# Kernel optimization log

Hardware: AMD Instinct MI355X
Metric: run time of the kernel (lower is better)

Reference implementation:

```python
import jax, jax.numpy as jnp
import numpy as np
import math

H = 1024
N_HEADS = 16
B, S = 2, 2048

def setup_inputs() -> dict:
    key = jax.random.key(0)
    ks = jax.random.split(key, 10)
    s = 0.02
    inp = {
        "x": jax.random.normal(ks[0], (B, S, H), dtype=jnp.float32),
        "attention_mask": jnp.zeros((B, 1, 1, S), dtype=jnp.float32),
        "Wq": jax.random.normal(ks[1], (H, H), dtype=jnp.float32) * s,
        "bq": jnp.zeros((H,), dtype=jnp.float32),
        "Wk": jax.random.normal(ks[2], (H, H), dtype=jnp.float32) * s,
        "bk": jnp.zeros((H,), dtype=jnp.float32),
        "Wv": jax.random.normal(ks[3], (H, H), dtype=jnp.float32) * s,
        "bv": jnp.zeros((H,), dtype=jnp.float32),
        "Wo": jax.random.normal(ks[4], (H, H), dtype=jnp.float32) * s,
        "bo": jnp.zeros((H,), dtype=jnp.float32),
    }
    return inp

def reference(x, attention_mask, Wq, bq, Wk, bk, Wv, bv, Wo, bo):
    b, s, h = x.shape
    n = N_HEADS
    d = h // n
    scale = 1.0 / math.sqrt(h / n)
    # Linear projections (torch Linear: x @ W.T + b)
    q = (x @ Wq.T + bq).reshape(b, s, n, d).transpose(0, 2, 1, 3)  # [b,n,s,d]
    k = (x @ Wk.T + bk).reshape(b, s, n, d).transpose(0, 2, 1, 3)
    v = (x @ Wv.T + bv).reshape(b, s, n, d).transpose(0, 2, 1, 3)
    scores = jnp.einsum("bnqd,bnkd->bnqk", q, k) * scale + attention_mask
    probs = jax.nn.softmax(scores, axis=-1)
    attn = jnp.einsum("bnqk,bnkd->bnqd", probs, v)
    attn = attn.transpose(0, 2, 1, 3).reshape(b, s, h)
    return attn @ Wo.T + bo
```

## Files before the change

kernel.cpp:

```cpp
#include <hip/hip_runtime.h>

typedef __bf16 bf16;
typedef __bf16 bf16x8 __attribute__((ext_vector_type(8)));
typedef __bf16 bf16x4 __attribute__((ext_vector_type(4)));
typedef float f32x4 __attribute__((ext_vector_type(4)));
typedef float f32x16 __attribute__((ext_vector_type(16)));
typedef unsigned int u32;
typedef u32 u32x4 __attribute__((ext_vector_type(4)));
typedef const u32 __attribute__((address_space(1)))* gp1_t;
typedef u32 __attribute__((address_space(3)))* lp3_t;

constexpr int Hdim = 1024;
constexpr int SEQ  = 2048;
constexpr int NB   = 2;
constexpr int NHEAD = 16;
constexpr int DHEAD = 64;
constexpr int MR = NB * SEQ;
constexpr float LOG2E = 1.4426950408889634f;
constexpr float QSCALE = 0.125f * LOG2E;

__device__ __forceinline__ float fexp2(float x) { return __builtin_amdgcn_exp2f(x); }

__device__ __forceinline__ void gld16(const void* g, void* l) {
  __builtin_amdgcn_global_load_lds((gp1_t)g, (lp3_t)l, 16, 0, 0);
}

__device__ __forceinline__ u32 cvtpk_bf16(float lo, float hi) {
  u32 r;
  asm("v_cvt_pk_bf16_f32 %0, %1, %2" : "=v"(r) : "v"(lo), "v"(hi));
  return r;
}

__global__ __launch_bounds__(256) void cvt_all_k(
    const float* __restrict__ x, const float* __restrict__ Wq, const float* __restrict__ Wk,
    const float* __restrict__ Wv, const float* __restrict__ Wo, const float* __restrict__ mask,
    bf16* __restrict__ xb, bf16* __restrict__ wqkv, bf16* __restrict__ wob,
    float* __restrict__ maskS) {
  const int n8x = MR * Hdim / 8;
  const int n8w = Hdim * Hdim / 8;
  int i = blockIdx.x * 256 + threadIdx.x;
  if (i >= n8x + 4 * n8w) {
    int o = i - (n8x + 4 * n8w);
    const float4* p = reinterpret_cast<const float4*>(mask) + (size_t)o * 2;
    float4 a = p[0], b = p[1];
    a.x *= LOG2E; a.y *= LOG2E; a.z *= LOG2E; a.w *= LOG2E;
    b.x *= LOG2E; b.y *= LOG2E; b.z *= LOG2E; b.w *= LOG2E;
    float4* q = reinterpret_cast<float4*>(maskS) + (size_t)o * 2;
    q[0] = a; q[1] = b;
    return;
  }
  const float* src;
  bf16* dst;
  int slot;
  if (i < n8x) {
    src = x; dst = xb; slot = i;
  } else {
    int j = i - n8x;
    int w = j >> 17;
    int o = j & (n8w - 1);
    if (w == 0)      { src = Wq; dst = wqkv;            }
    else if (w == 1) { src = Wk; dst = wqkv + (size_t)Hdim * Hdim;     }
    else if (w == 2) { src = Wv; dst = wqkv + (size_t)2 * Hdim * Hdim; }
    else             { src = Wo; dst = wob;             }
    slot = o;
  }
  const float4* p = reinterpret_cast<const float4*>(src) + (size_t)slot * 2;
  float4 a = p[0], b = p[1];
  bf16x8 o8;
  o8[0] = (bf16)a.x; o8[1] = (bf16)a.y; o8[2] = (bf16)a.z; o8[3] = (bf16)a.w;
  o8[4] = (bf16)b.x; o8[5] = (bf16)b.y; o8[6] = (bf16)b.z; o8[7] = (bf16)b.w;
  reinterpret_cast<bf16x8*>(dst)[slot] = o8;
}

__global__ __launch_bounds__(256) void qkv_gemm_k(
    const bf16* __restrict__ A, const bf16* __restrict__ Bw,
    const float* __restrict__ bq, const float* __restrict__ bk, const float* __restrict__ bv,
    bf16* __restrict__ Qw, bf16* __restrict__ Kw, bf16* __restrict__ VTw)
{
  __shared__ __align__(16) bf16 As[3][128][32];
  __shared__ __align__(16) bf16 Bs[3][128][32];

  const int t = threadIdx.x;
  const int lane = t & 63, wave = t >> 6;
  const int ql = lane & 15, g = lane >> 4;
  const int wr = wave >> 1, wc = wave & 1;
  const int row0 = blockIdx.x * 128;
  const int col0 = blockIdx.y * 128;
  const int z = blockIdx.y >> 3;
  const float* bias = (z == 0) ? bq : (z == 1) ? bk : bv;
  const int rsl = (g ^ ((ql >> 1) & 3)) * 8;

  f32x4 acc[4][4] = {};

#define STAGE_QKV(buf, kt)                                                        \
  {                                                                               \
    _Pragma("unroll")                                                             \
    for (int i = 0; i < 2; ++i) {                                                 \
      int c = i * 256 + t;                                                        \
      int r = c >> 2, sp = c & 3;                                                 \
      int sl = (sp ^ ((r >> 1) & 3)) << 3;                                        \
      gld16(&A[(size_t)(row0 + r) * Hdim + (kt) + sl], (char*)&As[buf][0][0] + c * 16); \
      gld16(&Bw[(size_t)(col0 + r) * Hdim + (kt) + sl], (char*)&Bs[buf][0][0] + c * 16); \
    }                                                                             \
  }

  constexpr int NT = Hdim / 32;
  STAGE_QKV(0, 0);
  STAGE_QKV(1, 32);

  int cur = 0;
  for (int it = 0; it < NT; ++it) {
    if (it + 2 < NT) {
      int stg = cur + 2; if (stg >= 3) stg -= 3;
      STAGE_QKV(stg, (it + 2) * 32);
      asm volatile("s_waitcnt vmcnt(8)" ::: "memory");
    } else if (it + 1 < NT) {
      asm volatile("s_waitcnt vmcnt(4)" ::: "memory");
    } else {
      asm volatile("s_waitcnt vmcnt(0)" ::: "memory");
    }
    __builtin_amdgcn_s_barrier();

    bf16x8 af[4], bfr[4];
#pragma unroll
    for (int m = 0; m < 4; ++m)
      af[m] = *reinterpret_cast<const bf16x8*>(&As[cur][wr * 64 + m * 16 + ql][rsl]);
#pragma unroll
    for (int n = 0; n < 4; ++n)
      bfr[n] = *reinterpret_cast<const bf16x8*>(&Bs[cur][wc * 64 + n * 16 + ql][rsl]);
#pragma unroll
    for (int m = 0; m < 4; ++m)
#pragma unroll
      for (int n = 0; n < 4; ++n)
        acc[m][n] = __builtin_amdgcn_mfma_f32_16x16x32_bf16(af[m], bfr[n], acc[m][n], 0, 0, 0);

    __builtin_amdgcn_s_barrier();
    cur = (cur + 1 == 3) ? 0 : cur + 1;
  }
#undef STAGE_QKV

  const float oscale = (z == 0) ? QSCALE : 1.0f;
#pragma unroll
  for (int m = 0; m < 4; ++m) {
#pragma unroll
    for (int n = 0; n < 4; ++n) {
#pragma unroll
      for (int r = 0; r < 4; ++r) {
        int gi = row0 + wr * 64 + m * 16 + g * 4 + r;
        int gj = col0 + wc * 64 + n * 16 + ql;
        int j1 = gj & (Hdim - 1);
        float v = (acc[m][n][r] + bias[j1]) * oscale;
        int b = gi >> 11, s = gi & (SEQ - 1);
        int hh = j1 >> 6, dd = j1 & 63;
        if (z == 0)
          Qw[((size_t)(b * NHEAD + hh) * SEQ + s) * DHEAD + dd] = (bf16)v;
        else if (z == 1)
          Kw[((size_t)(b * NHEAD + hh) * SEQ + s) * DHEAD + dd] = (bf16)v;
        else
          VTw[((size_t)(b * NHEAD + hh) * DHEAD + dd) * SEQ + s] = (bf16)v;
      }
    }
  }
}

__global__ __launch_bounds__(256, 2) void attn_fwd_k(
    const bf16* __restrict__ Q, const bf16* __restrict__ K,
    const bf16* __restrict__ VT, const float* __restrict__ maskS,
    bf16* __restrict__ Out)
{
  const int head = blockIdx.x;
  const int qt = blockIdx.y;
  const int b = head >> 4;
  const int hh = head & 15;
  const int t = threadIdx.x, lane = t & 63, wave = t >> 6;
  const int q = lane & 31, h = lane >> 5;

  __shared__ __align__(16) bf16 Ks[3][64][64];
  __shared__ __align__(16) bf16 VTs[3][64][64];
  __shared__ __align__(16) float Ms[SEQ];

  const bf16* Qh  = Q  + (size_t)head * SEQ * DHEAD;
  const bf16* Kh  = K  + (size_t)head * SEQ * DHEAD;
  const bf16* VTh = VT + (size_t)head * DHEAD * SEQ;
  const float* mrow = maskS + (size_t)b * SEQ;

  const int q0w = qt * 128 + wave * 32;

  bf16x8 qf[4];
#pragma unroll
  for (int s = 0; s < 4; ++s)
    qf[s] = *reinterpret_cast<const bf16x8*>(&Qh[(size_t)(q0w + q) * DHEAD + s * 16 + 8 * h]);

  f32x16 accT[2] = {};
  f32x4 psum4 = {0.f, 0.f, 0.f, 0.f};

#define STAGE_KV(buf, tile)                                                       \
  {                                                                               \
    const int nb0 = (tile) * 64;                                                  \
    _Pragma("unroll")                                                             \
    for (int i = 0; i < 2; ++i) {                                                 \
      int c = i * 256 + t, r = c >> 3, sp = c & 7, sl = sp ^ (r & 7);             \
      gld16(&Kh[(size_t)(nb0 + r) * DHEAD + sl * 8], (char*)&Ks[buf][0][0] + c * 16); \
      gld16(&VTh[(size_t)r * SEQ + nb0 + sl * 8], (char*)&VTs[buf][0][0] + c * 16);   \
    }                                                                             \
  }

  constexpr int NT = SEQ / 64;
#pragma unroll
  for (int i = 0; i < 2; ++i) {
    int c = i * 256 + t;
    gld16(&mrow[c * 4], (char*)&Ms[0] + c * 16);
  }
  STAGE_KV(0, 0);
  STAGE_KV(1, 1);
  asm volatile("s_waitcnt vmcnt(4)" ::: "memory");
  __builtin_amdgcn_s_barrier();

  int cur = 0;
  for (int it = 0; it < NT; ++it) {
    if (it + 2 < NT) {
      int stg = cur + 2; if (stg >= 3) stg -= 3;
      STAGE_KV(stg, it + 2);
    }

    const char* ksb = (const char*)&Ks[cur][0][0];
    const char* vsb = (const char*)&VTs[cur][0][0];
    const int kb0 = it * 64;

    f32x16 sacc[2];
#pragma unroll
    for (int tt = 0; tt < 2; ++tt) {
#pragma unroll
      for (int s = 0; s < 4; ++s) {
        f32x4 m4 = *reinterpret_cast<const f32x4*>(&Ms[kb0 + 32 * tt + 8 * s + 4 * h]);
#pragma unroll
        for (int r = 0; r < 4; ++r) sacc[tt][s * 4 + r] = m4[r];
      }
    }

    __builtin_amdgcn_s_setprio(1);
#pragma unroll
    for (int tt = 0; tt < 2; ++tt) {
      const int row = 32 * tt + q;
      const int rsw = (row & 7) << 4;
#pragma unroll
      for (int s = 0; s < 4; ++s) {
        bf16x8 kf = *reinterpret_cast<const bf16x8*>(ksb + row * 128 + ((32 * s + 16 * h) ^ rsw));
        sacc[tt] = __builtin_amdgcn_mfma_f32_32x32x16_bf16(kf, qf[s], sacc[tt], 0, 0, 0);
      }
    }
    __builtin_amdgcn_s_setprio(0);

    float pe[2][16];
#pragma unroll
    for (int tt = 0; tt < 2; ++tt)
#pragma unroll
      for (int i = 0; i < 16; ++i) {
        pe[tt][i] = fexp2(sacc[tt][i]);
        psum4[i & 3] += pe[tt][i];
      }

    u32x4 pw[4];
#pragma unroll
    for (int m = 0; m < 4; ++m) {
      const int tt = m >> 1, mi = (m & 1) * 8;
      u32 w0a = cvtpk_bf16(pe[tt][mi + 0], pe[tt][mi + 1]);
      u32 w0b = cvtpk_bf16(pe[tt][mi + 2], pe[tt][mi + 3]);
      u32 w1a = cvtpk_bf16(pe[tt][mi + 4], pe[tt][mi + 5]);
      u32 w1b = cvtpk_bf16(pe[tt][mi + 6], pe[tt][mi + 7]);
      asm("v_permlane32_swap_b32 %0, %1" : "+v"(w0a), "+v"(w1a));
      asm("v_permlane32_swap_b32 %0, %1" : "+v"(w0b), "+v"(w1b));
      pw[m][0] = w0a; pw[m][1] = w0b; pw[m][2] = w1a; pw[m][3] = w1b;
    }

    __builtin_amdgcn_s_setprio(1);
#pragma unroll
    for (int td = 0; td < 2; ++td) {
      const int row = 32 * td + q;
      const int rsw = (row & 7) << 4;
#pragma unroll
      for (int m = 0; m < 4; ++m) {
        bf16x8 vf = *reinterpret_cast<const bf16x8*>(vsb + row * 128 + ((32 * m + 16 * h) ^ rsw));
        bf16x8 pf = __builtin_bit_cast(bf16x8, pw[m]);
        accT[td] = __builtin_amdgcn_mfma_f32_32x32x16_bf16(vf, pf, accT[td], 0, 0, 0);
      }
    }
    __builtin_amdgcn_s_setprio(0);

    if (it + 2 < NT)      asm volatile("s_waitcnt vmcnt(4)" ::: "memory");
    else if (it + 1 < NT) asm volatile("s_waitcnt vmcnt(0)" ::: "memory");
    __builtin_amdgcn_s_barrier();
    cur = (cur + 1 == 3) ? 0 : cur + 1;
  }
#undef STAGE_KV

  float l = (psum4[0] + psum4[1]) + (psum4[2] + psum4[3]);
  l += __shfl_xor(l, 32);
  const float inv = 1.0f / l;

  char* slab = (char*)&Ks[0][0][0] + wave * 4096;
  const int qsw = (q & 7) << 4;
#pragma unroll
  for (int td = 0; td < 2; ++td)
#pragma unroll
    for (int s = 0; s < 4; ++s) {
      bf16x4 o4;
#pragma unroll
      for (int r = 0; r < 4; ++r) o4[r] = (bf16)(accT[td][s * 4 + r] * inv);
      *reinterpret_cast<bf16x4*>(slab + q * 128 + (((32 * td + 8 * s + 4 * h) * 2) ^ qsw)) = o4;
    }
  asm volatile("s_waitcnt lgkmcnt(0)" ::: "memory");
#pragma unroll
  for (int i = 0; i < 4; ++i) {
    const int row = i * 8 + (lane >> 3);
    bf16x8 v = *reinterpret_cast<const bf16x8*>(slab + row * 128 + (((lane & 7) << 4) ^ ((row & 7) << 4)));
    *reinterpret_cast<bf16x8*>(&Out[((size_t)(b * SEQ) + q0w + row) * Hdim + hh * 64 + (lane & 7) * 8]) = v;
  }
}

__global__ __launch_bounds__(256) void out_gemm_k(
    const bf16* __restrict__ A, const bf16* __restrict__ Bm,
    const float* __restrict__ bias, float* __restrict__ C)
{
  __shared__ __align__(16) bf16 As[3][128][32];
  __shared__ __align__(16) bf16 Bs[3][64][32];

  const int t = threadIdx.x;
  const int lane = t & 63, wave = t >> 6;
  const int ql = lane & 15, g = lane >> 4;
  const int wr = wave >> 1, wc = wave & 1;
  const int row0 = blockIdx.x * 128;
  const int col0 = blockIdx.y * 64;
  const int rsl = (g ^ ((ql >> 1) & 3)) * 8;

  f32x4 acc[4][2] = {};

#define STAGE_OUT(buf, kt)                                                        \
  {                                                                               \
    _Pragma("unroll")                                                             \
    for (int i = 0; i < 2; ++i) {                                                 \
      int c = i * 256 + t;                                                        \
      int r = c >> 2, sp = c & 3;                                                 \
      int sl = (sp ^ ((r >> 1) & 3)) << 3;                                        \
      gld16(&A[(size_t)(row0 + r) * Hdim + (kt) + sl], (char*)&As[buf][0][0] + c * 16); \
    }                                                                             \
    {                                                                             \
      int c = t;                                                                  \
      int r = c >> 2, sp = c & 3;                                                 \
      int sl = (sp ^ ((r >> 1) & 3)) << 3;                                        \
      gld16(&Bm[(size_t)(col0 + r) * Hdim + (kt) + sl], (char*)&Bs[buf][0][0] + c * 16); \
    }                                                                             \
  }

  constexpr int NT = Hdim / 32;
  STAGE_OUT(0, 0);
  STAGE_OUT(1, 32);

  int cur = 0;
  for (int it = 0; it < NT; ++it) {
    if (it + 2 < NT) {
      int stg = cur + 2; if (stg >= 3) stg -= 3;
      STAGE_OUT(stg, (it + 2) * 32);
      asm volatile("s_waitcnt vmcnt(6)" ::: "memory");
    } else if (it + 1 < NT) {
      asm volatile("s_waitcnt vmcnt(3)" ::: "memory");
    } else {
      asm volatile("s_waitcnt vmcnt(0)" ::: "memory");
    }
    __builtin_amdgcn_s_barrier();

    bf16x8 af[4], bfr[2];
#pragma unroll
    for (int m = 0; m < 4; ++m)
      af[m] = *reinterpret_cast<const bf16x8*>(&As[cur][wr * 64 + m * 16 + ql][rsl]);
#pragma unroll
    for (int n = 0; n < 2; ++n)
      bfr[n] = *reinterpret_cast<const bf16x8*>(&Bs[cur][wc * 32 + n * 16 + ql][rsl]);
#pragma unroll
    for (int m = 0; m < 4; ++m)
#pragma unroll
      for (int n = 0; n < 2; ++n)
        acc[m][n] = __builtin_amdgcn_mfma_f32_16x16x32_bf16(af[m], bfr[n], acc[m][n], 0, 0, 0);

    __builtin_amdgcn_s_barrier();
    cur = (cur + 1 == 3) ? 0 : cur + 1;
  }
#undef STAGE_OUT

#pragma unroll
  for (int m = 0; m < 4; ++m)
#pragma unroll
    for (int n = 0; n < 2; ++n)
#pragma unroll
      for (int r = 0; r < 4; ++r) {
        int gi = row0 + wr * 64 + m * 16 + g * 4 + r;
        int gj = col0 + wc * 32 + n * 16 + ql;
        C[(size_t)gi * Hdim + gj] = acc[m][n][r] + bias[gj];
      }
}

extern "C" void kernel_launch(void* const* d_in, const int* in_sizes, int n_in,
                              void* d_out, int out_size, void* d_ws, size_t ws_size,
                              hipStream_t stream) {
  const float* x    = (const float*)d_in[0];
  const float* mask = (const float*)d_in[1];
  const float* Wq   = (const float*)d_in[2];
  const float* bq   = (const float*)d_in[3];
  const float* Wk   = (const float*)d_in[4];
  const float* bk   = (const float*)d_in[5];
  const float* Wv   = (const float*)d_in[6];
  const float* bv   = (const float*)d_in[7];
  const float* Wo   = (const float*)d_in[8];
  const float* bo   = (const float*)d_in[9];
  float* out = (float*)d_out;

  bf16* xb   = (bf16*)d_ws;
  const size_t big = (size_t)MR * Hdim;
  bf16* wqkv = xb + big;
  bf16* wob  = wqkv + (size_t)3 * Hdim * Hdim;
  bf16* qw   = wob + (size_t)Hdim * Hdim;
  bf16* kw   = qw + big;
  bf16* vtw  = kw + big;
  bf16* attnb = vtw + big;
  float* maskS = (float*)(attnb + big);

  const int nslots = MR * Hdim / 8 + 4 * (Hdim * Hdim / 8) + NB * SEQ / 8;
  cvt_all_k<<<nslots / 256, 256, 0, stream>>>(x, Wq, Wk, Wv, Wo, mask, xb, wqkv, wob, maskS);

  qkv_gemm_k<<<dim3(MR / 128, 3 * Hdim / 128), 256, 0, stream>>>(
      xb, wqkv, bq, bk, bv, qw, kw, vtw);

  attn_fwd_k<<<dim3(NB * NHEAD, SEQ / 128), 256, 0, stream>>>(qw, kw, vtw, maskS, attnb);

  out_gemm_k<<<dim3(MR / 128, Hdim / 64), 256, 0, stream>>>(attnb, wob, bo, out);
}
```

Measured before the change: 118.2 us.

## Store mask as bf16, simplify QKV GEMM staging, raise attention occupancy

Three changes land together. The additive mask is now stored in bf16 instead of fp32, which halves its LDS footprint in the attention kernel, and the attention kernel's launch bounds go from 2 to 3 blocks per CU to allow more occupancy. Separately, the QKV GEMM drops its 3-stage prefetch pipeline for a single 64-wide K tile, loaded synchronously each iteration with an XOR-swizzled layout, which cuts LDS use but exposes global load latency. The bf16 mask loses precision for non-zero mask values, and the tighter launch bound may cause register spills.

```diff
diff --git a/kernel.cpp b/kernel.cpp
--- a/kernel.cpp
+++ b/kernel.cpp
@@ -35,26 +35,16 @@
     const float* __restrict__ x, const float* __restrict__ Wq, const float* __restrict__ Wk,
     const float* __restrict__ Wv, const float* __restrict__ Wo, const float* __restrict__ mask,
     bf16* __restrict__ xb, bf16* __restrict__ wqkv, bf16* __restrict__ wob,
-    float* __restrict__ maskS) {
+    bf16* __restrict__ maskB) {
   const int n8x = MR * Hdim / 8;
   const int n8w = Hdim * Hdim / 8;
   int i = blockIdx.x * 256 + threadIdx.x;
-  if (i >= n8x + 4 * n8w) {
-    int o = i - (n8x + 4 * n8w);
-    const float4* p = reinterpret_cast<const float4*>(mask) + (size_t)o * 2;
-    float4 a = p[0], b = p[1];
-    a.x *= LOG2E; a.y *= LOG2E; a.z *= LOG2E; a.w *= LOG2E;
-    b.x *= LOG2E; b.y *= LOG2E; b.z *= LOG2E; b.w *= LOG2E;
-    float4* q = reinterpret_cast<float4*>(maskS) + (size_t)o * 2;
-    q[0] = a; q[1] = b;
-    return;
-  }
   const float* src;
   bf16* dst;
   int slot;
   if (i < n8x) {
     src = x; dst = xb; slot = i;
-  } else {
+  } else if (i < n8x + 4 * n8w) {
     int j = i - n8x;
     int w = j >> 17;
     int o = j & (n8w - 1);
@@ -63,6 +53,17 @@
     else if (w == 2) { src = Wv; dst = wqkv + (size_t)2 * Hdim * Hdim; }
     else             { src = Wo; dst = wob;             }
     slot = o;
+  } else {
+    int o = i - (n8x + 4 * n8w);
+    const float4* p = reinterpret_cast<const float4*>(mask) + (size_t)o * 2;
+    float4 a = p[0], b = p[1];
+    bf16x8 o8;
+    o8[0] = (bf16)(a.x * LOG2E); o8[1] = (bf16)(a.y * LOG2E);
+    o8[2] = (bf16)(a.z * LOG2E); o8[3] = (bf16)(a.w * LOG2E);
+    o8[4] = (bf16)(b.x * LOG2E); o8[5] = (bf16)(b.y * LOG2E);
+    o8[6] = (bf16)(b.z * LOG2E); o8[7] = (bf16)(b.w * LOG2E);
+    reinterpret_cast<bf16x8*>(maskB)[o] = o8;
+    return;
   }
   const float4* p = reinterpret_cast<const float4*>(src) + (size_t)slot * 2;
   float4 a = p[0], b = p[1];
@@ -77,8 +78,8 @@
     const float* __restrict__ bq, const float* __restrict__ bk, const float* __restrict__ bv,
     bf16* __restrict__ Qw, bf16* __restrict__ Kw, bf16* __restrict__ VTw)
 {
-  __shared__ __align__(16) bf16 As[3][128][32];
-  __shared__ __align__(16) bf16 Bs[3][128][32];
+  __shared__ __align__(16) bf16 As[128][64];
+  __shared__ __align__(16) bf16 Bs[128][64];
 
   const int t = threadIdx.x;
   const int lane = t & 63, wave = t >> 6;
@@ -88,56 +89,43 @@
   const int col0 = blockIdx.y * 128;
   const int z = blockIdx.y >> 3;
   const float* bias = (z == 0) ? bq : (z == 1) ? bk : bv;
-  const int rsl = (g ^ ((ql >> 1) & 3)) * 8;
 
   f32x4 acc[4][4] = {};
 
-#define STAGE_QKV(buf, kt)                                                        \
-  {                                                                               \
-    _Pragma("unroll")                                                             \
-    for (int i = 0; i < 2; ++i) {                                                 \
-      int c = i * 256 + t;                                                        \
-      int r = c >> 2, sp = c & 3;                                                 \
-      int sl = (sp ^ ((r >> 1) & 3)) << 3;                                        \
-      gld16(&A[(size_t)(row0 + r) * Hdim + (kt) + sl], (char*)&As[buf][0][0] + c * 16); \
-      gld16(&Bw[(size_t)(col0 + r) * Hdim + (kt) + sl], (char*)&Bs[buf][0][0] + c * 16); \
-    }                                                                             \
-  }
-
-  constexpr int NT = Hdim / 32;
-  STAGE_QKV(0, 0);
-  STAGE_QKV(1, 32);
-
-  int cur = 0;
-  for (int it = 0; it < NT; ++it) {
-    if (it + 2 < NT) {
-      int stg = cur + 2; if (stg >= 3) stg -= 3;
-      STAGE_QKV(stg, (it + 2) * 32);
-      asm volatile("s_waitcnt vmcnt(8)" ::: "memory");
-    } else if (it + 1 < NT) {
-      asm volatile("s_waitcnt vmcnt(4)" ::: "memory");
-    } else {
-      asm volatile("s_waitcnt vmcnt(0)" ::: "memory");
-    }
+  for (int kt = 0; kt < Hdim; kt += 64) {
     __builtin_amdgcn_s_barrier();
-
-    bf16x8 af[4], bfr[4];
-#pragma unroll
-    for (int m = 0; m < 4; ++m)
-      af[m] = *reinterpret_cast<const bf16x8*>(&As[cur][wr * 64 + m * 16 + ql][rsl]);
-#pragma unroll
-    for (int n = 0; n < 4; ++n)
-      bfr[n] = *reinterpret_cast<const bf16x8*>(&Bs[cur][wc * 64 + n * 16 + ql][rsl]);
-#pragma unroll
-    for (int m = 0; m < 4; ++m)
-#pragma unroll
-      for (int n = 0; n < 4; ++n)
-        acc[m][n] = __builtin_amdgcn_mfma_f32_16x16x32_bf16(af[m], bfr[n], acc[m][n], 0, 0, 0);
-
+#pragma unroll
+    for (int i = 0; i < 4; ++i) {
+      int c = i * 256 + t;
+      int r = c >> 3, sp = c & 7, sl = (sp ^ (r & 7)) << 3;
+      gld16(&A[(size_t)(row0 + r) * Hdim + kt + sl], (char*)&As[0][0] + c * 16);
+      gld16(&Bw[(size_t)(col0 + r) * Hdim + kt + sl], (char*)&Bs[0][0] + c * 16);
+    }
+    asm volatile("s_waitcnt vmcnt(0)" ::: "memory");
     __builtin_amdgcn_s_barrier();
-    cur = (cur + 1 == 3) ? 0 : cur + 1;
-  }
-#undef STAGE_QKV
+
+#pragma unroll
+    for (int kk = 0; kk < 2; ++kk) {
+      bf16x8 af[4], bfr[4];
+#pragma unroll
+      for (int m = 0; m < 4; ++m) {
+        const int row = wr * 64 + m * 16 + ql;
+        af[m] = *reinterpret_cast<const bf16x8*>(
+            (const char*)&As[0][0] + row * 128 + ((kk * 64 + g * 16) ^ ((row & 7) << 4)));
+      }
+#pragma unroll
+      for (int n = 0; n < 4; ++n) {
+        const int row = wc * 64 + n * 16 + ql;
+        bfr[n] = *reinterpret_cast<const bf16x8*>(
+            (const char*)&Bs[0][0] + row * 128 + ((kk * 64 + g * 16) ^ ((row & 7) << 4)));
+      }
+#pragma unroll
+      for (int m = 0; m < 4; ++m)
+#pragma unroll
+        for (int n = 0; n < 4; ++n)
+          acc[m][n] = __builtin_amdgcn_mfma_f32_16x16x32_bf16(af[m], bfr[n], acc[m][n], 0, 0, 0);
+    }
+  }
 
   const float oscale = (z == 0) ? QSCALE : 1.0f;
 #pragma unroll
@@ -163,9 +151,9 @@
   }
 }
 
-__global__ __launch_bounds__(256, 2) void attn_fwd_k(
+__global__ __launch_bounds__(256, 3) void attn_fwd_k(
     const bf16* __restrict__ Q, const bf16* __restrict__ K,
-    const bf16* __restrict__ VT, const float* __restrict__ maskS,
+    const bf16* __restrict__ VT, const bf16* __restrict__ maskB,
     bf16* __restrict__ Out)
 {
   const int head = blockIdx.x;
@@ -177,12 +165,12 @@
 
   __shared__ __align__(16) bf16 Ks[3][64][64];
   __shared__ __align__(16) bf16 VTs[3][64][64];
-  __shared__ __align__(16) float Ms[SEQ];
+  __shared__ __align__(16) bf16 Ms[SEQ];
 
   const bf16* Qh  = Q  + (size_t)head * SEQ * DHEAD;
   const bf16* Kh  = K  + (size_t)head * SEQ * DHEAD;
   const bf16* VTh = VT + (size_t)head * DHEAD * SEQ;
-  const float* mrow = maskS + (size_t)b * SEQ;
+  const bf16* mrow = maskB + (size_t)b * SEQ;
 
   const int q0w = qt * 128 + wave * 32;
 
@@ -206,11 +194,7 @@
   }
 
   constexpr int NT = SEQ / 64;
-#pragma unroll
-  for (int i = 0; i < 2; ++i) {
-    int c = i * 256 + t;
-    gld16(&mrow[c * 4], (char*)&Ms[0] + c * 16);
-  }
+  gld16(&mrow[t * 8], (char*)&Ms[0] + t * 16);
   STAGE_KV(0, 0);
   STAGE_KV(1, 1);
   asm volatile("s_waitcnt vmcnt(4)" ::: "memory");
@@ -232,9 +216,9 @@
     for (int tt = 0; tt < 2; ++tt) {
 #pragma unroll
       for (int s = 0; s < 4; ++s) {
-        f32x4 m4 = *reinterpret_cast<const f32x4*>(&Ms[kb0 + 32 * tt + 8 * s + 4 * h]);
-#pragma unroll
-        for (int r = 0; r < 4; ++r) sacc[tt][s * 4 + r] = m4[r];
+        bf16x4 m4 = *reinterpret_cast<const bf16x4*>(&Ms[kb0 + 32 * tt + 8 * s + 4 * h]);
+#pragma unroll
+        for (int r = 0; r < 4; ++r) sacc[tt][s * 4 + r] = (float)m4[r];
       }
     }
 
@@ -422,15 +406,15 @@
   bf16* kw   = qw + big;
   bf16* vtw  = kw + big;
   bf16* attnb = vtw + big;
-  float* maskS = (float*)(attnb + big);
+  bf16* maskB = attnb + big;
 
   const int nslots = MR * Hdim / 8 + 4 * (Hdim * Hdim / 8) + NB * SEQ / 8;
-  cvt_all_k<<<nslots / 256, 256, 0, stream>>>(x, Wq, Wk, Wv, Wo, mask, xb, wqkv, wob, maskS);
+  cvt_all_k<<<nslots / 256, 256, 0, stream>>>(x, Wq, Wk, Wv, Wo, mask, xb, wqkv, wob, maskB);
 
   qkv_gemm_k<<<dim3(MR / 128, 3 * Hdim / 128), 256, 0, stream>>>(
       xb, wqkv, bq, bk, bv, qw, kw, vtw);
 
-  attn_fwd_k<<<dim3(NB * NHEAD, SEQ / 128), 256, 0, stream>>>(qw, kw, vtw, maskS, attnb);
+  attn_fwd_k<<<dim3(NB * NHEAD, SEQ / 128), 256, 0, stream>>>(qw, kw, vtw, maskB, attnb);
 
   out_gemm_k<<<dim3(MR / 128, Hdim / 64), 256, 0, stream>>>(attnb, wob, bo, out);
 }
```

After: 124.3 us. 5.1% more time.

## Enlarge QKV GEMM row tile, store mask as bf16, raise attention occupancy

Applied to the files above, without the earlier changes.

The QKV projection GEMM tile grows from 128 to 256 rows per block, with 8x4 MFMA accumulators per wave. This doubles reuse of the weight tiles, at the cost of more registers and half as many blocks (16x24). The additive mask is converted to bf16 during preprocessing, which halves its LDS footprint and load traffic in the attention kernel but reduces mask precision. The attention kernel's launch bounds ask for 3 blocks per CU instead of 2, which may force register spilling.

```diff
diff --git a/kernel.cpp b/kernel.cpp
--- a/kernel.cpp
+++ b/kernel.cpp
@@ -35,26 +35,16 @@
     const float* __restrict__ x, const float* __restrict__ Wq, const float* __restrict__ Wk,
     const float* __restrict__ Wv, const float* __restrict__ Wo, const float* __restrict__ mask,
     bf16* __restrict__ xb, bf16* __restrict__ wqkv, bf16* __restrict__ wob,
-    float* __restrict__ maskS) {
+    bf16* __restrict__ maskB) {
   const int n8x = MR * Hdim / 8;
   const int n8w = Hdim * Hdim / 8;
   int i = blockIdx.x * 256 + threadIdx.x;
-  if (i >= n8x + 4 * n8w) {
-    int o = i - (n8x + 4 * n8w);
-    const float4* p = reinterpret_cast<const float4*>(mask) + (size_t)o * 2;
-    float4 a = p[0], b = p[1];
-    a.x *= LOG2E; a.y *= LOG2E; a.z *= LOG2E; a.w *= LOG2E;
-    b.x *= LOG2E; b.y *= LOG2E; b.z *= LOG2E; b.w *= LOG2E;
-    float4* q = reinterpret_cast<float4*>(maskS) + (size_t)o * 2;
-    q[0] = a; q[1] = b;
-    return;
-  }
   const float* src;
   bf16* dst;
   int slot;
   if (i < n8x) {
     src = x; dst = xb; slot = i;
-  } else {
+  } else if (i < n8x + 4 * n8w) {
     int j = i - n8x;
     int w = j >> 17;
     int o = j & (n8w - 1);
@@ -63,6 +53,17 @@
     else if (w == 2) { src = Wv; dst = wqkv + (size_t)2 * Hdim * Hdim; }
     else             { src = Wo; dst = wob;             }
     slot = o;
+  } else {
+    int o = i - (n8x + 4 * n8w);
+    const float4* p = reinterpret_cast<const float4*>(mask) + (size_t)o * 2;
+    float4 a = p[0], b = p[1];
+    bf16x8 o8;
+    o8[0] = (bf16)(a.x * LOG2E); o8[1] = (bf16)(a.y * LOG2E);
+    o8[2] = (bf16)(a.z * LOG2E); o8[3] = (bf16)(a.w * LOG2E);
+    o8[4] = (bf16)(b.x * LOG2E); o8[5] = (bf16)(b.y * LOG2E);
+    o8[6] = (bf16)(b.z * LOG2E); o8[7] = (bf16)(b.w * LOG2E);
+    reinterpret_cast<bf16x8*>(maskB)[o] = o8;
+    return;
   }
   const float4* p = reinterpret_cast<const float4*>(src) + (size_t)slot * 2;
   float4 a = p[0], b = p[1];
@@ -77,29 +78,35 @@
     const float* __restrict__ bq, const float* __restrict__ bk, const float* __restrict__ bv,
     bf16* __restrict__ Qw, bf16* __restrict__ Kw, bf16* __restrict__ VTw)
 {
-  __shared__ __align__(16) bf16 As[3][128][32];
+  __shared__ __align__(16) bf16 As[3][256][32];
   __shared__ __align__(16) bf16 Bs[3][128][32];
 
   const int t = threadIdx.x;
   const int lane = t & 63, wave = t >> 6;
   const int ql = lane & 15, g = lane >> 4;
   const int wr = wave >> 1, wc = wave & 1;
-  const int row0 = blockIdx.x * 128;
+  const int row0 = blockIdx.x * 256;
   const int col0 = blockIdx.y * 128;
   const int z = blockIdx.y >> 3;
   const float* bias = (z == 0) ? bq : (z == 1) ? bk : bv;
   const int rsl = (g ^ ((ql >> 1) & 3)) * 8;
 
-  f32x4 acc[4][4] = {};
+  f32x4 acc[8][4] = {};
 
 #define STAGE_QKV(buf, kt)                                                        \
   {                                                                               \
+    _Pragma("unroll")                                                             \
+    for (int i = 0; i < 4; ++i) {                                                 \
+      int c = i * 256 + t;                                                        \
+      int r = c >> 2, sp = c & 3;                                                 \
+      int sl = (sp ^ ((r >> 1) & 3)) << 3;                                        \
+      gld16(&A[(size_t)(row0 + r) * Hdim + (kt) + sl], (char*)&As[buf][0][0] + c * 16); \
+    }                                                                             \
     _Pragma("unroll")                                                             \
     for (int i = 0; i < 2; ++i) {                                                 \
       int c = i * 256 + t;                                                        \
       int r = c >> 2, sp = c & 3;                                                 \
       int sl = (sp ^ ((r >> 1) & 3)) << 3;                                        \
-      gld16(&A[(size_t)(row0 + r) * Hdim + (kt) + sl], (char*)&As[buf][0][0] + c * 16); \
       gld16(&Bw[(size_t)(col0 + r) * Hdim + (kt) + sl], (char*)&Bs[buf][0][0] + c * 16); \
     }                                                                             \
   }
@@ -113,23 +120,23 @@
     if (it + 2 < NT) {
       int stg = cur + 2; if (stg >= 3) stg -= 3;
       STAGE_QKV(stg, (it + 2) * 32);
-      asm volatile("s_waitcnt vmcnt(8)" ::: "memory");
+      asm volatile("s_waitcnt vmcnt(12)" ::: "memory");
     } else if (it + 1 < NT) {
-      asm volatile("s_waitcnt vmcnt(4)" ::: "memory");
+      asm volatile("s_waitcnt vmcnt(6)" ::: "memory");
     } else {
       asm volatile("s_waitcnt vmcnt(0)" ::: "memory");
     }
     __builtin_amdgcn_s_barrier();
 
-    bf16x8 af[4], bfr[4];
-#pragma unroll
-    for (int m = 0; m < 4; ++m)
-      af[m] = *reinterpret_cast<const bf16x8*>(&As[cur][wr * 64 + m * 16 + ql][rsl]);
+    bf16x8 af[8], bfr[4];
+#pragma unroll
+    for (int m = 0; m < 8; ++m)
+      af[m] = *reinterpret_cast<const bf16x8*>(&As[cur][wr * 128 + m * 16 + ql][rsl]);
 #pragma unroll
     for (int n = 0; n < 4; ++n)
       bfr[n] = *reinterpret_cast<const bf16x8*>(&Bs[cur][wc * 64 + n * 16 + ql][rsl]);
 #pragma unroll
-    for (int m = 0; m < 4; ++m)
+    for (int m = 0; m < 8; ++m)
 #pragma unroll
       for (int n = 0; n < 4; ++n)
         acc[m][n] = __builtin_amdgcn_mfma_f32_16x16x32_bf16(af[m], bfr[n], acc[m][n], 0, 0, 0);
@@ -141,12 +148,12 @@
 
   const float oscale = (z == 0) ? QSCALE : 1.0f;
 #pragma unroll
-  for (int m = 0; m < 4; ++m) {
+  for (int m = 0; m < 8; ++m) {
 #pragma unroll
     for (int n = 0; n < 4; ++n) {
 #pragma unroll
       for (int r = 0; r < 4; ++r) {
-        int gi = row0 + wr * 64 + m * 16 + g * 4 + r;
+        int gi = row0 + wr * 128 + m * 16 + g * 4 + r;
         int gj = col0 + wc * 64 + n * 16 + ql;
         int j1 = gj & (Hdim - 1);
         float v = (acc[m][n][r] + bias[j1]) * oscale;
@@ -163,9 +170,9 @@
   }
 }
 
-__global__ __launch_bounds__(256, 2) void attn_fwd_k(
+__global__ __launch_bounds__(256, 3) void attn_fwd_k(
     const bf16* __restrict__ Q, const bf16* __restrict__ K,
-    const bf16* __restrict__ VT, const float* __restrict__ maskS,
+    const bf16* __restrict__ VT, const bf16* __restrict__ maskB,
     bf16* __restrict__ Out)
 {
   const int head = blockIdx.x;
@@ -177,12 +184,12 @@
 
   __shared__ __align__(16) bf16 Ks[3][64][64];
   __shared__ __align__(16) bf16 VTs[3][64][64];
-  __shared__ __align__(16) float Ms[SEQ];
+  __shared__ __align__(16) bf16 Ms[SEQ];
 
   const bf16* Qh  = Q  + (size_t)head * SEQ * DHEAD;
   const bf16* Kh  = K  + (size_t)head * SEQ * DHEAD;
   const bf16* VTh = VT + (size_t)head * DHEAD * SEQ;
-  const float* mrow = maskS + (size_t)b * SEQ;
+  const bf16* mrow = maskB + (size_t)b * SEQ;
 
   const int q0w = qt * 128 + wave * 32;
 
@@ -206,11 +213,7 @@
   }
 
   constexpr int NT = SEQ / 64;
-#pragma unroll
-  for (int i = 0; i < 2; ++i) {
-    int c = i * 256 + t;
-    gld16(&mrow[c * 4], (char*)&Ms[0] + c * 16);
-  }
+  gld16(&mrow[t * 8], (char*)&Ms[0] + t * 16);
   STAGE_KV(0, 0);
   STAGE_KV(1, 1);
   asm volatile("s_waitcnt vmcnt(4)" ::: "memory");
@@ -232,9 +235,9 @@
     for (int tt = 0; tt < 2; ++tt) {
 #pragma unroll
       for (int s = 0; s < 4; ++s) {
-        f32x4 m4 = *reinterpret_cast<const f32x4*>(&Ms[kb0 + 32 * tt + 8 * s + 4 * h]);
-#pragma unroll
-        for (int r = 0; r < 4; ++r) sacc[tt][s * 4 + r] = m4[r];
+        bf16x4 m4 = *reinterpret_cast<const bf16x4*>(&Ms[kb0 + 32 * tt + 8 * s + 4 * h]);
+#pragma unroll
+        for (int r = 0; r < 4; ++r) sacc[tt][s * 4 + r] = (float)m4[r];
       }
     }
 
@@ -422,15 +425,15 @@
   bf16* kw   = qw + big;
   bf16* vtw  = kw + big;
   bf16* attnb = vtw + big;
-  float* maskS = (float*)(attnb + big);
+  bf16* maskB = attnb + big;
 
   const int nslots = MR * Hdim / 8 + 4 * (Hdim * Hdim / 8) + NB * SEQ / 8;
-  cvt_all_k<<<nslots / 256, 256, 0, stream>>>(x, Wq, Wk, Wv, Wo, mask, xb, wqkv, wob, maskS);
-
-  qkv_gemm_k<<<dim3(MR / 128, 3 * Hdim / 128), 256, 0, stream>>>(
+  cvt_all_k<<<nslots / 256, 256, 0, stream>>>(x, Wq, Wk, Wv, Wo, mask, xb, wqkv, wob, maskB);
+
+  qkv_gemm_k<<<dim3(MR / 256, 3 * Hdim / 128), 256, 0, stream>>>(
       xb, wqkv, bq, bk, bv, qw, kw, vtw);
 
-  attn_fwd_k<<<dim3(NB * NHEAD, SEQ / 128), 256, 0, stream>>>(qw, kw, vtw, maskS, attnb);
+  attn_fwd_k<<<dim3(NB * NHEAD, SEQ / 128), 256, 0, stream>>>(qw, kw, vtw, maskB, attnb);
 
   out_gemm_k<<<dim3(MR / 128, Hdim / 64), 256, 0, stream>>>(attnb, wob, bo, out);
 }
```

Measured after the change: 169.6 us. 43.5% more time.
